# Kernel optimization log

Measured on AMD Instinct MI355X. Metric: run time of the kernel, lower is better.

Reference implementation:

```python
import jax, jax.numpy as jnp
import numpy as np
from jax import lax

BATCH = 512
SEQ = 512
VOCAB = 1000
EMB_DIM = 100
UNITS = 64


def setup_inputs() -> dict:
    key = jax.random.key(0)
    k_tok, k_emb, k_wxh, k_whh, k_wout = jax.random.split(key, 5)
    inputs = jax.random.randint(k_tok, (BATCH, SEQ), 0, VOCAB, dtype=jnp.int32)
    emb = jax.random.normal(k_emb, (VOCAB, EMB_DIM), dtype=jnp.float32) * 0.05
    Wxh = jax.random.normal(k_wxh, (EMB_DIM, UNITS), dtype=jnp.float32) * (1.0 / np.sqrt(EMB_DIM))
    # Keras recurrent_initializer is orthogonal; a scaled normal is fine for a numeric reference
    Whh = jax.random.normal(k_whh, (UNITS, UNITS), dtype=jnp.float32) * (1.0 / np.sqrt(UNITS))
    b = jnp.zeros((UNITS,), dtype=jnp.float32)
    Wout = jax.random.normal(k_wout, (UNITS, 1), dtype=jnp.float32) * (1.0 / np.sqrt(UNITS))
    bout = jnp.zeros((1,), dtype=jnp.float32)
    return {"inputs": inputs, "emb": emb, "Wxh": Wxh, "Whh": Whh, "b": b, "Wout": Wout, "bout": bout}


def reference(inputs, emb, Wxh, Whh, b, Wout, bout):
    # Embedding lookup: [B, T] int -> [B, T, D]
    x = emb[inputs]
    # Pre-project inputs once (x_t @ Wxh for all t) to keep the scan body minimal
    xproj = jnp.einsum('btd,du->btu', x, Wxh) + b  # [B, T, U]
    xs = jnp.swapaxes(xproj, 0, 1)  # [T, B, U] time-major for scan

    def step(h, xt):
        h_new = jnp.tanh(xt + h @ Whh)
        return h_new, None

    h0 = jnp.zeros((inputs.shape[0], Whh.shape[0]), dtype=emb.dtype)
    hT, _ = lax.scan(step, h0, xs)  # return_sequences=False -> final state only
    logits = hT @ Wout + bout  # [B, 1]
    return jax.nn.sigmoid(logits)
```

## Files before the change

kernel.cpp:

```cpp
#include <hip/hip_runtime.h>

#define BATCH 512
#define SEQ   512
#define VOCAB 1000
#define EMB   100
#define UNITS 64
#define SC    2.88539008177792681f

typedef float v2f __attribute__((ext_vector_type(2)));

__global__ __launch_bounds__(64) void proj_kernel(
    const float* __restrict__ emb, const float* __restrict__ Wxh,
    const float* __restrict__ bias, const float* __restrict__ Whh,
    float* __restrict__ P) {
  const int v = blockIdx.x;
  const int u = threadIdx.x;
  const float* e = emb + v * EMB;
  float acc = bias[u];
#pragma unroll 5
  for (int d = 0; d < EMB; ++d) acc += e[d] * Wxh[d * UNITS + u];
  float csum = 0.f;
#pragma unroll 8
  for (int i = 0; i < UNITS; ++i) csum += Whh[i * UNITS + u];
  P[v * UNITS + u] = SC * (acc + csum);
}

#define DPP_I(src, ctrl) __builtin_amdgcn_update_dpp(0, (src), (ctrl), 0xF, 0xF, true)

#define GATHER_ROW(v_, g_)                                          \
  do {                                                              \
    g_[0] = DPP_I((v_), 0x00);             \
    g_[1] = DPP_I((v_), 0x55);             \
    g_[2] = DPP_I((v_), 0xAA);             \
    g_[3] = DPP_I((v_), 0xFF);             \
    g_[4]  = DPP_I(g_[0], 0x124); g_[5]  = DPP_I(g_[1], 0x124);     \
    g_[6]  = DPP_I(g_[2], 0x124); g_[7]  = DPP_I(g_[3], 0x124);     \
    g_[8]  = DPP_I(g_[0], 0x128); g_[9]  = DPP_I(g_[1], 0x128);     \
    g_[10] = DPP_I(g_[2], 0x128); g_[11] = DPP_I(g_[3], 0x128);     \
    g_[12] = DPP_I(g_[0], 0x12C); g_[13] = DPP_I(g_[1], 0x12C);     \
    g_[14] = DPP_I(g_[2], 0x12C); g_[15] = DPP_I(g_[3], 0x12C);     \
  } while (0)

__device__ __forceinline__ float sw16(float v, bool sel) {
  int x = __float_as_int(v), y = x;
  asm volatile("s_nop 1\n\tv_permlane16_swap_b32 %0, %1" : "+v"(x), "+v"(y));
  return sel ? __int_as_float(x) : __int_as_float(y);
}
__device__ __forceinline__ float sw32(float v, bool sel) {
  int x = __float_as_int(v), y = x;
  asm volatile("s_nop 1\n\tv_permlane32_swap_b32 %0, %1" : "+v"(x), "+v"(y));
  return sel ? __int_as_float(x) : __int_as_float(y);
}

__global__ __launch_bounds__(64)
__attribute__((amdgpu_waves_per_eu(1, 1)))
void scan_kernel(
    const int* __restrict__ tok, const float* __restrict__ P,
    const float* __restrict__ Whh, const float* __restrict__ Wout,
    const float* __restrict__ bout, float* __restrict__ out) {
  const int row  = blockIdx.x;
  const int lane = threadIdx.x;

  int gcal[16];
  GATHER_ROW(lane, gcal);

  int x16 = lane, y16 = lane;
  asm volatile("s_nop 1\n\tv_permlane16_swap_b32 %0, %1" : "+v"(x16), "+v"(y16));
  const bool sel16 = (x16 == (lane ^ 16));
  int x32 = lane, y32 = lane;
  asm volatile("s_nop 1\n\tv_permlane32_swap_b32 %0, %1" : "+v"(x32), "+v"(y32));
  const bool sel32 = (x32 == (lane ^ 32));

  const int c0 = lane, c1 = lane ^ 16, c2 = lane ^ 32, c3 = lane ^ 48;
  v2f w0[8], w1[8], w2[8], w3[8];
#pragma unroll
  for (int s = 0; s < 8; ++s) {
    const int i0 = gcal[2 * s] * UNITS, i1 = gcal[2 * s + 1] * UNITS;
    float t00 = -2.f * SC * Whh[i0 + c0], t01 = -2.f * SC * Whh[i1 + c0];
    float t10 = -2.f * SC * Whh[i0 + c1], t11 = -2.f * SC * Whh[i1 + c1];
    float t20 = -2.f * SC * Whh[i0 + c2], t21 = -2.f * SC * Whh[i1 + c2];
    float t30 = -2.f * SC * Whh[i0 + c3], t31 = -2.f * SC * Whh[i1 + c3];
    asm volatile("" : "+v"(t00), "+v"(t01), "+v"(t10), "+v"(t11));
    asm volatile("" : "+v"(t20), "+v"(t21), "+v"(t30), "+v"(t31));
    w0[s].x = t00; w0[s].y = t01;  w1[s].x = t10; w1[s].y = t11;
    w2[s].x = t20; w2[s].y = t21;  w3[s].x = t30; w3[s].y = t31;
  }

  int tokv[SEQ / 64];
  const int* trow = tok + (long)row * SEQ;
#pragma unroll
  for (int c = 0; c < SEQ / 64; ++c) {
    int t = trow[c * 64 + lane] * UNITS;
    asm volatile("" : "+v"(t));
    tokv[c] = t;
  }

  float r = 0.5f;

  float a0 = P[(long)__builtin_amdgcn_readlane(tokv[0], 0) + lane];
  float a1 = P[(long)__builtin_amdgcn_readlane(tokv[0], 1) + lane];

#pragma unroll
  for (int c = 0; c < SEQ / 64; ++c) {
#pragma unroll
    for (int tt = 0; tt < 64; ++tt) {
      float a_cur = a0;
      a0 = a1;
      int tkn = __builtin_amdgcn_readlane(tokv[c], (tt + 2) & 63);
      a1 = P[(long)tkn + lane];

      int gi[16];
      GATHER_ROW(__float_as_int(r), gi);

      v2f acc0, acc1 = {0.f, 0.f}, acc2 = {0.f, 0.f}, acc3 = {0.f, 0.f};
      acc0.x = a_cur; acc0.y = 0.f;
#pragma unroll
      for (int s = 0; s < 8; ++s) {
        v2f gp;
        gp.x = __int_as_float(gi[2 * s]);
        gp.y = __int_as_float(gi[2 * s + 1]);
        acc0 += gp * w0[s];
        acc1 += gp * w1[s];
        acc2 += gp * w2[s];
        acc3 += gp * w3[s];
      }
      float p0 = acc0.x + acc0.y;
      float p1 = acc1.x + acc1.y;
      float p2 = acc2.x + acc2.y;
      float p3 = acc3.x + acc3.y;

      float s1 = p0 + sw16(p1, sel16);
      float s2 = p2 + sw16(p3, sel16);
      float yv = s1 + sw32(s2, sel32);

      float ex; asm("v_exp_f32 %0, %1" : "=v"(ex) : "v"(yv));
      r = __builtin_amdgcn_rcpf(ex + 1.f);
    }
    if (c + 1 < SEQ / 64) {
      a0 = P[(long)__builtin_amdgcn_readlane(tokv[c + 1], 0) + lane];
      a1 = P[(long)__builtin_amdgcn_readlane(tokv[c + 1], 1) + lane];
    }
  }

  float h = __builtin_fmaf(-2.f, r, 1.f);
  float p = h * Wout[lane];
#pragma unroll
  for (int off = 32; off > 0; off >>= 1) p += __shfl_xor(p, off);
  if (lane == 0) out[row] = 1.f / (1.f + __expf(-(p + bout[0])));
}

extern "C" void kernel_launch(void* const* d_in, const int* in_sizes, int n_in,
                              void* d_out, int out_size, void* d_ws, size_t ws_size,
                              hipStream_t stream) {
  const int*   tok  = (const int*)  d_in[0];
  const float* emb  = (const float*)d_in[1];
  const float* Wxh  = (const float*)d_in[2];
  const float* Whh  = (const float*)d_in[3];
  const float* bias = (const float*)d_in[4];
  const float* Wout = (const float*)d_in[5];
  const float* bout = (const float*)d_in[6];
  float* out = (float*)d_out;

  float* P = (float*)d_ws;

  proj_kernel<<<VOCAB, 64, 0, stream>>>(emb, Wxh, bias, Whh, P);
  scan_kernel<<<BATCH, 64, 0, stream>>>(tok, P, Whh, Wout, bout, out);
}
```

Baseline: 99.47 us.

## Process two batch rows per wavefront to interleave independent recurrence chains

Each scan wavefront now advances two batch rows simultaneously, interleaving their DPP gathers, packed FMAs, lane swaps and exp/rcp so the two dependency chains hide each other's latency. The grid is halved accordingly. Token indices are now read per step from memory with a short prefetch instead of being preloaded into VGPRs and extracted with readlane, and the asm volatile qualifiers on the permlane swaps are dropped to allow scheduling. The change risks higher per-wave instruction count and register pressure, with fewer waves in flight.

```diff
diff --git a/kernel.cpp b/kernel.cpp
--- a/kernel.cpp
+++ b/kernel.cpp
@@ -29,10 +29,8 @@
 
 #define GATHER_ROW(v_, g_)                                          \
   do {                                                              \
-    g_[0] = DPP_I((v_), 0x00);             \
-    g_[1] = DPP_I((v_), 0x55);             \
-    g_[2] = DPP_I((v_), 0xAA);             \
-    g_[3] = DPP_I((v_), 0xFF);             \
+    g_[0] = DPP_I((v_), 0x00);  g_[1] = DPP_I((v_), 0x55);          \
+    g_[2] = DPP_I((v_), 0xAA);  g_[3] = DPP_I((v_), 0xFF);          \
     g_[4]  = DPP_I(g_[0], 0x124); g_[5]  = DPP_I(g_[1], 0x124);     \
     g_[6]  = DPP_I(g_[2], 0x124); g_[7]  = DPP_I(g_[3], 0x124);     \
     g_[8]  = DPP_I(g_[0], 0x128); g_[9]  = DPP_I(g_[1], 0x128);     \
@@ -41,14 +39,34 @@
     g_[14] = DPP_I(g_[2], 0x12C); g_[15] = DPP_I(g_[3], 0x12C);     \
   } while (0)
 
+#define GATHER2(vA_, gA_, vB_, gB_)                                          \
+  do {                                                                       \
+    gA_[0] = DPP_I((vA_), 0x00);  gB_[0] = DPP_I((vB_), 0x00);               \
+    gA_[1] = DPP_I((vA_), 0x55);  gB_[1] = DPP_I((vB_), 0x55);               \
+    gA_[2] = DPP_I((vA_), 0xAA);  gB_[2] = DPP_I((vB_), 0xAA);               \
+    gA_[3] = DPP_I((vA_), 0xFF);  gB_[3] = DPP_I((vB_), 0xFF);               \
+    gA_[4]  = DPP_I(gA_[0], 0x124); gB_[4]  = DPP_I(gB_[0], 0x124);          \
+    gA_[5]  = DPP_I(gA_[1], 0x124); gB_[5]  = DPP_I(gB_[1], 0x124);          \
+    gA_[6]  = DPP_I(gA_[2], 0x124); gB_[6]  = DPP_I(gB_[2], 0x124);          \
+    gA_[7]  = DPP_I(gA_[3], 0x124); gB_[7]  = DPP_I(gB_[3], 0x124);          \
+    gA_[8]  = DPP_I(gA_[0], 0x128); gB_[8]  = DPP_I(gB_[0], 0x128);          \
+    gA_[9]  = DPP_I(gA_[1], 0x128); gB_[9]  = DPP_I(gB_[1], 0x128);          \
+    gA_[10] = DPP_I(gA_[2], 0x128); gB_[10] = DPP_I(gB_[2], 0x128);          \
+    gA_[11] = DPP_I(gA_[3], 0x128); gB_[11] = DPP_I(gB_[3], 0x128);          \
+    gA_[12] = DPP_I(gA_[0], 0x12C); gB_[12] = DPP_I(gB_[0], 0x12C);          \
+    gA_[13] = DPP_I(gA_[1], 0x12C); gB_[13] = DPP_I(gB_[1], 0x12C);          \
+    gA_[14] = DPP_I(gA_[2], 0x12C); gB_[14] = DPP_I(gB_[2], 0x12C);          \
+    gA_[15] = DPP_I(gA_[3], 0x12C); gB_[15] = DPP_I(gB_[3], 0x12C);          \
+  } while (0)
+
 __device__ __forceinline__ float sw16(float v, bool sel) {
   int x = __float_as_int(v), y = x;
-  asm volatile("s_nop 1\n\tv_permlane16_swap_b32 %0, %1" : "+v"(x), "+v"(y));
+  asm("s_nop 1\n\tv_permlane16_swap_b32 %0, %1" : "+v"(x), "+v"(y));
   return sel ? __int_as_float(x) : __int_as_float(y);
 }
 __device__ __forceinline__ float sw32(float v, bool sel) {
   int x = __float_as_int(v), y = x;
-  asm volatile("s_nop 1\n\tv_permlane32_swap_b32 %0, %1" : "+v"(x), "+v"(y));
+  asm("s_nop 1\n\tv_permlane32_swap_b32 %0, %1" : "+v"(x), "+v"(y));
   return sel ? __int_as_float(x) : __int_as_float(y);
 }
 
@@ -58,8 +76,9 @@
     const int* __restrict__ tok, const float* __restrict__ P,
     const float* __restrict__ Whh, const float* __restrict__ Wout,
     const float* __restrict__ bout, float* __restrict__ out) {
-  const int row  = blockIdx.x;
   const int lane = threadIdx.x;
+  const int rowA = blockIdx.x * 2;
+  const int rowB = rowA + 1;
 
   int gcal[16];
   GATHER_ROW(lane, gcal);
@@ -86,67 +105,80 @@
     w2[s].x = t20; w2[s].y = t21;  w3[s].x = t30; w3[s].y = t31;
   }
 
-  int tokv[SEQ / 64];
-  const int* trow = tok + (long)row * SEQ;
+  const int* trA = tok + (long)rowA * SEQ;
+  const int* trB = tok + (long)rowB * SEQ;
+
+  float rr_A = 0.5f, rr_B = 0.5f;
+
+  int tkAc = trA[2], tkAn = trA[3];
+  int tkBc = trB[2], tkBn = trB[3];
+  float a0A = P[(long)trA[0] * UNITS + lane];
+  float a1A = P[(long)trA[1] * UNITS + lane];
+  float a0B = P[(long)trB[0] * UNITS + lane];
+  float a1B = P[(long)trB[1] * UNITS + lane];
+
+#pragma unroll 8
+  for (int t = 0; t < SEQ; ++t) {
+    float aCA = a0A; a0A = a1A;
+    float aCB = a0B; a0B = a1B;
+    a1A = P[(long)tkAc * UNITS + lane];
+    a1B = P[(long)tkBc * UNITS + lane];
+    const int nidx = (t + 4 < SEQ) ? t + 4 : SEQ - 1;
+    tkAc = tkAn; tkAn = trA[nidx];
+    tkBc = tkBn; tkBn = trB[nidx];
+
+    int giA[16], giB[16];
+    GATHER2(__float_as_int(rr_A), giA, __float_as_int(rr_B), giB);
+
+    v2f qA0, qA1 = {0.f, 0.f}, qA2 = {0.f, 0.f}, qA3 = {0.f, 0.f};
+    v2f qB0, qB1 = {0.f, 0.f}, qB2 = {0.f, 0.f}, qB3 = {0.f, 0.f};
+    qA0.x = aCA; qA0.y = 0.f;
+    qB0.x = aCB; qB0.y = 0.f;
 #pragma unroll
-  for (int c = 0; c < SEQ / 64; ++c) {
-    int t = trow[c * 64 + lane] * UNITS;
-    asm volatile("" : "+v"(t));
-    tokv[c] = t;
-  }
-
-  float r = 0.5f;
-
-  float a0 = P[(long)__builtin_amdgcn_readlane(tokv[0], 0) + lane];
-  float a1 = P[(long)__builtin_amdgcn_readlane(tokv[0], 1) + lane];
-
+    for (int s = 0; s < 8; ++s) {
+      v2f gA, gB;
+      gA.x = __int_as_float(giA[2 * s]);
+      gA.y = __int_as_float(giA[2 * s + 1]);
+      gB.x = __int_as_float(giB[2 * s]);
+      gB.y = __int_as_float(giB[2 * s + 1]);
+      qA0 += gA * w0[s];  qB0 += gB * w0[s];
+      qA1 += gA * w1[s];  qB1 += gB * w1[s];
+      qA2 += gA * w2[s];  qB2 += gB * w2[s];
+      qA3 += gA * w3[s];  qB3 += gB * w3[s];
+    }
+    float pA0 = qA0.x + qA0.y, pB0 = qB0.x + qB0.y;
+    float pA1 = qA1.x + qA1.y, pB1 = qB1.x + qB1.y;
+    float pA2 = qA2.x + qA2.y, pB2 = qB2.x + qB2.y;
+    float pA3 = qA3.x + qA3.y, pB3 = qB3.x + qB3.y;
+
+    float s1A = pA0 + sw16(pA1, sel16);
+    float s1B = pB0 + sw16(pB1, sel16);
+    float s2A = pA2 + sw16(pA3, sel16);
+    float s2B = pB2 + sw16(pB3, sel16);
+    float yA = s1A + sw32(s2A, sel32);
+    float yB = s1B + sw32(s2B, sel32);
+
+    float exA; asm("v_exp_f32 %0, %1" : "=v"(exA) : "v"(yA));
+    float exB; asm("v_exp_f32 %0, %1" : "=v"(exB) : "v"(yB));
+    rr_A = __builtin_amdgcn_rcpf(exA + 1.f);
+    rr_B = __builtin_amdgcn_rcpf(exB + 1.f);
+  }
+
+  float hA = __builtin_fmaf(-2.f, rr_A, 1.f);
+  float hB = __builtin_fmaf(-2.f, rr_B, 1.f);
+  float wl = Wout[lane];
+  float pA = hA * wl;
+  float pB = hB * wl;
 #pragma unroll
-  for (int c = 0; c < SEQ / 64; ++c) {
-#pragma unroll
-    for (int tt = 0; tt < 64; ++tt) {
-      float a_cur = a0;
-      a0 = a1;
-      int tkn = __builtin_amdgcn_readlane(tokv[c], (tt + 2) & 63);
-      a1 = P[(long)tkn + lane];
-
-      int gi[16];
-      GATHER_ROW(__float_as_int(r), gi);
-
-      v2f acc0, acc1 = {0.f, 0.f}, acc2 = {0.f, 0.f}, acc3 = {0.f, 0.f};
-      acc0.x = a_cur; acc0.y = 0.f;
-#pragma unroll
-      for (int s = 0; s < 8; ++s) {
-        v2f gp;
-        gp.x = __int_as_float(gi[2 * s]);
-        gp.y = __int_as_float(gi[2 * s + 1]);
-        acc0 += gp * w0[s];
-        acc1 += gp * w1[s];
-        acc2 += gp * w2[s];
-        acc3 += gp * w3[s];
-      }
-      float p0 = acc0.x + acc0.y;
-      float p1 = acc1.x + acc1.y;
-      float p2 = acc2.x + acc2.y;
-      float p3 = acc3.x + acc3.y;
-
-      float s1 = p0 + sw16(p1, sel16);
-      float s2 = p2 + sw16(p3, sel16);
-      float yv = s1 + sw32(s2, sel32);
-
-      float ex; asm("v_exp_f32 %0, %1" : "=v"(ex) : "v"(yv));
-      r = __builtin_amdgcn_rcpf(ex + 1.f);
-    }
-    if (c + 1 < SEQ / 64) {
-      a0 = P[(long)__builtin_amdgcn_readlane(tokv[c + 1], 0) + lane];
-      a1 = P[(long)__builtin_amdgcn_readlane(tokv[c + 1], 1) + lane];
-    }
-  }
-
-  float h = __builtin_fmaf(-2.f, r, 1.f);
-  float p = h * Wout[lane];
-#pragma unroll
-  for (int off = 32; off > 0; off >>= 1) p += __shfl_xor(p, off);
-  if (lane == 0) out[row] = 1.f / (1.f + __expf(-(p + bout[0])));
+  for (int off = 32; off > 0; off >>= 1) {
+    pA += __shfl_xor(pA, off);
+    pB += __shfl_xor(pB, off);
+  }
+  if (lane == 0) {
+    float b0 = bout[0];
+    out[rowA] = 1.f / (1.f + __expf(-(pA + b0)));
+    out[rowB] = 1.f / (1.f + __expf(-(pB + b0)));
+  }
 }
 
 extern "C" void kernel_launch(void* const* d_in, const int* in_sizes, int n_in,
@@ -164,5 +196,5 @@
   float* P = (float*)d_ws;
 
   proj_kernel<<<VOCAB, 64, 0, stream>>>(emb, Wxh, bias, Whh, P);
-  scan_kernel<<<BATCH, 64, 0, stream>>>(tok, P, Whh, Wout, bout, out);
-}
+  scan_kernel<<<BATCH / 2, 64, 0, stream>>>(tok, P, Whh, Wout, bout, out);
+}
```

Measured after the change: 179.0 us. 80.0% more time.
